# Performance work log

Measured on AMD Instinct MI355X. Metric: run time of the kernel, lower is better.

Reference implementation:

```python
import jax, jax.numpy as jnp
import numpy as np

B, T, E = 8, 2048, 1024
H = 16
HD = E // H            # per-head hidden_dim = 64
DFF = 4 * E
DC = T // 512          # decay_constant = 4
EPS = 1e-5


def setup_inputs() -> dict:
    key = jax.random.key(0)
    ks = jax.random.split(key, 8)
    return {
        "x": jax.random.normal(ks[0], (B, T, E), jnp.float32),
        # per-head input projections (Linear(dim, hidden_dim) x H)
        "w_proj": jax.random.normal(ks[1], (H, E, HD), jnp.float32) / np.sqrt(E),
        "b_proj": jnp.zeros((H, HD), jnp.float32),
        # causal mixing weights: first H//2 heads are Col-repeat, last H//2 Row-repeat
        "mix_w": jax.random.normal(ks[2], (H, T), jnp.float32),
        "mix_b": jnp.zeros((H, T), jnp.float32),
        "decay": jnp.ones((H,), jnp.float32),   # decay_value params (init ones as in torch)
        "out_w": jax.random.normal(ks[3], (E, E), jnp.float32) / np.sqrt(E),
        "out_b": jnp.zeros((E,), jnp.float32),
        "ln1_g": jnp.ones((E,), jnp.float32),
        "ln1_b": jnp.zeros((E,), jnp.float32),
        "ln2_g": jnp.ones((E,), jnp.float32),
        "ln2_b": jnp.zeros((E,), jnp.float32),
        "ff_w1": jax.random.normal(ks[4], (E, DFF), jnp.float32) / np.sqrt(E),
        "ff_b1": jnp.zeros((DFF,), jnp.float32),
        "ff_w2": jax.random.normal(ks[5], (DFF, E), jnp.float32) / np.sqrt(DFF),
        "ff_b2": jnp.zeros((E,), jnp.float32),
        "index": 0,
    }


def _layernorm(x, g, b):
    mu = jnp.mean(x, -1, keepdims=True)
    var = jnp.var(x, -1, keepdims=True)
    return (x - mu) * jax.lax.rsqrt(var + EPS) * g + b


def _mix_matrices(mix_w, decay):
    # Col heads: M[i,j] = v[j] * d**((j-i)/DC) for j>=i else 0
    # Row heads: M[i,j] = v[i] * d**((j-i)/DC) for j>=i else 0
    i = jnp.arange(T)[:, None]
    j = jnp.arange(T)[None, :]
    d = jnp.clip(decay, 0.9, 1.0)                                   # (H,)
    expo = (j - i).astype(jnp.float32) / DC                         # (T,T)
    dec = d[:, None, None] ** expo                                  # (H,T,T)
    causal = (j >= i)
    half = H // 2
    Mcol = jnp.where(causal, mix_w[:half, None, :] * dec[:half], 0.0)
    Mrow = jnp.where(causal, mix_w[half:, :, None] * dec[half:], 0.0)
    return jnp.concatenate([Mcol, Mrow], axis=0)                    # (H,T,T)


def reference(x, w_proj, b_proj, mix_w, mix_b, decay, out_w, out_b,
              ln1_g, ln1_b, ln2_g, ln2_b, ff_w1, ff_b1, ff_w2, ff_b2, index):
    # ---- token-mixing sub-block (parallel path of MixedRepeatHeads) ----
    res = x
    h = _layernorm(x, ln1_g, ln1_b)
    # per-head projection: (B,T,E) x (H,E,HD) -> (B,H,T,HD)
    p = jnp.einsum('bte,hef->bhtf', h, w_proj) + b_proj[:, None, :]
    M = _mix_matrices(mix_w, decay)
    # causal decay mixing along time: out[b,h,s,f] = sum_t p[b,h,t,f] * M[h,t,s]
    mixed = jnp.einsum('bhtf,hts->bhsf', p, M) + mix_b[None, :, :, None]
    # concat heads along feature dim -> (B,T,E)
    mixed = mixed.transpose(0, 2, 1, 3).reshape(B, T, E)
    mixed = mixed @ out_w + out_b
    x = mixed + res
    # ---- feed-forward sub-block ----
    res = x
    h = _layernorm(x, ln2_g, ln2_b)
    h = jax.nn.gelu(h @ ff_w1 + ff_b1) @ ff_w2 + ff_b2
    return h + res
```

## Files before the change

kernel.cpp:

```cpp
#include <hip/hip_runtime.h>


#define TT 2048
#define EE 1024
#define HHD 64
#define MROWS 16384
#define SC_L 64

typedef __bf16 bf16x8 __attribute__((ext_vector_type(8)));
typedef float f32x4 __attribute__((ext_vector_type(4)));
typedef unsigned short u16;
typedef unsigned int u32;
typedef u16 u16x8 __attribute__((ext_vector_type(8)));

__device__ __forceinline__ u16 f2bf(float f) {
  u32 u = __builtin_bit_cast(u32, f);
  u += 0x7FFFu + ((u >> 16) & 1u);
  return (u16)(u >> 16);
}
__device__ __forceinline__ float bf2f(u16 s) {
  u32 u = ((u32)s) << 16;
  return __builtin_bit_cast(float, u);
}
__device__ __forceinline__ float gelu_f(float x) {
  float x2 = x * x;
  float e = -1.5957691216057308f * x * __builtin_fmaf(0.044715f, x2, 1.0f);
  return x * __builtin_amdgcn_rcpf(1.0f + __expf(e));
}
__device__ __forceinline__ void gload_lds16(const void* g, void* l) {
  __builtin_amdgcn_global_load_lds(
      (const __attribute__((address_space(1))) u32*)g,
      (__attribute__((address_space(3))) u32*)l, 16, 0, 0);
}
__device__ __forceinline__ void wg_barrier() {
  asm volatile("" ::: "memory");
  __builtin_amdgcn_s_barrier();
  asm volatile("" ::: "memory");
}

__global__ __launch_bounds__(256) void transpose_to_bf16(
    const float* __restrict__ src, u16* __restrict__ dst, int R, int C,
    long sbs, long dbs) {
  __shared__ float tile[32][33];
  src += (long)blockIdx.z * sbs;
  dst += (long)blockIdx.z * dbs;
  int c0 = blockIdx.x * 32, r0 = blockIdx.y * 32;
  int tx = threadIdx.x, ty = threadIdx.y;
#pragma unroll
  for (int i = 0; i < 4; i++)
    tile[ty + i * 8][tx] = src[(long)(r0 + ty + i * 8) * C + c0 + tx];
  __syncthreads();
#pragma unroll
  for (int i = 0; i < 4; i++)
    dst[(long)(c0 + ty + i * 8) * R + r0 + tx] = f2bf(tile[tx][ty + i * 8]);
}

__global__ __launch_bounds__(256) void ln_to_bf16(
    const float* __restrict__ x, const float* __restrict__ gam,
    const float* __restrict__ bet, u16* __restrict__ y) {
  int row = blockIdx.x;
  int tid = threadIdx.x;
  float4 v = ((const float4*)x)[row * 256 + tid];
  float s = v.x + v.y + v.z + v.w;
  float s2 = v.x * v.x + v.y * v.y + v.z * v.z + v.w * v.w;
#pragma unroll
  for (int off = 1; off < 64; off <<= 1) {
    s += __shfl_xor(s, off);
    s2 += __shfl_xor(s2, off);
  }
  __shared__ float red[8];
  int w = tid >> 6;
  if ((tid & 63) == 0) { red[w] = s; red[4 + w] = s2; }
  __syncthreads();
  s = red[0] + red[1] + red[2] + red[3];
  s2 = red[4] + red[5] + red[6] + red[7];
  float mu = s * (1.0f / 1024.0f);
  float var = s2 * (1.0f / 1024.0f) - mu * mu;
  float rstd = rsqrtf(var + 1e-5f);
  int e0 = tid * 4;
  ushort4 o;
  o.x = f2bf((v.x - mu) * rstd * gam[e0 + 0] + bet[e0 + 0]);
  o.y = f2bf((v.y - mu) * rstd * gam[e0 + 1] + bet[e0 + 1]);
  o.z = f2bf((v.z - mu) * rstd * gam[e0 + 2] + bet[e0 + 2]);
  o.w = f2bf((v.w - mu) * rstd * gam[e0 + 3] + bet[e0 + 3]);
  ((ushort4*)y)[row * 256 + tid] = o;
}

template <int EPI>
__global__ __launch_bounds__(512, 1) void gemm256q(
    const u16* __restrict__ A, const u16* __restrict__ Bt,
    const float* __restrict__ bias, const float* __restrict__ res, void* outp,
    int M, int N, int K, int px, int gxp, int byper) {
  __shared__ u16 lds[65536];
  const int tid = threadIdx.x;
  const int w = tid >> 6, lane = tid & 63;
  const int wm = w >> 2, wn = w & 3;
  const int l15 = lane & 15, lk = lane >> 4;

  const int gx = (int)gridDim.x;
  const int bid = (int)blockIdx.y * gx + (int)blockIdx.x;
  const int xcd = bid & 7, i = bid >> 3;
  const int bx = (xcd % gxp) * px + (i % px);
  const int by = (xcd / gxp) * byper + (i / px);
  const int m0 = by * 256, n0 = bx * 256;

  const int srow = w * 16 + (lane >> 2);
  const int gslot = (lane & 3) ^ ((srow >> 1) & 3);
  const u16* aS = A + (size_t)(m0 + srow) * K + gslot * 8;
  const u16* aS2 = A + (size_t)(m0 + 128 + srow) * K +
                   (((lane & 3) ^ (((128 + srow) >> 1) & 3)) * 8);
  const u16* bS = Bt + (size_t)(n0 + srow) * K + gslot * 8;
  const u16* bS2 = Bt + (size_t)(n0 + 128 + srow) * K +
                   (((lane & 3) ^ (((128 + srow) >> 1) & 3)) * 8);

  f32x4 acc[8][4];
  const f32x4 z = {0.f, 0.f, 0.f, 0.f};
#pragma unroll
  for (int mi = 0; mi < 8; mi++)
#pragma unroll
    for (int ni = 0; ni < 4; ni++) acc[mi][ni] = z;

  const int sl = (lk ^ ((l15 >> 1) & 3)) * 8;
  const u32 ldsB = (u32)(uintptr_t)(void*)lds;
  const u32 aOffB = ldsB + (u32)(((wm * 128 + l15) * 32 + sl) * 2);
  const u32 bOffB = ldsB + 16384u + (u32)(((wn * 64 + l15) * 32 + sl) * 2);

#define STAGE(BUF, T_) { \
    u16* lb = lds + (BUF) * 16384 + w * 512; \
    const int kt = (T_) << 5; \
    gload_lds16(aS + kt, lb); \
    gload_lds16(aS2 + kt, lb + 4096); \
    gload_lds16(bS + kt, lb + 8192); \
    gload_lds16(bS2 + kt, lb + 12288); }

#define DS_RD(D, ADDR, OFF) \
    asm volatile("ds_read_b128 %0, %1 offset:" #OFF : "=v"(D) : "v"(ADDR))
#define WAITK(N_) { \
    asm volatile("s_waitcnt lgkmcnt(" #N_ ")" ::: "memory"); \
    __builtin_amdgcn_sched_barrier(0); }
#define MFMA4(MI, AF) { \
    acc[MI][0] = __builtin_amdgcn_mfma_f32_16x16x32_bf16(AF, bq0, acc[MI][0], 0, 0, 0); \
    acc[MI][1] = __builtin_amdgcn_mfma_f32_16x16x32_bf16(AF, bq1, acc[MI][1], 0, 0, 0); \
    acc[MI][2] = __builtin_amdgcn_mfma_f32_16x16x32_bf16(AF, bq2, acc[MI][2], 0, 0, 0); \
    acc[MI][3] = __builtin_amdgcn_mfma_f32_16x16x32_bf16(AF, bq3, acc[MI][3], 0, 0, 0); }

  const int nt = K >> 5;
  STAGE(0, 0);
  STAGE(1, 1);

  for (int t = 0; t < nt; ++t) {
    if (t + 2 < nt) {
      STAGE((t + 2) & 3, t + 2);
      asm volatile("s_waitcnt vmcnt(8)" ::: "memory");
    } else if (t + 1 < nt) {
      asm volatile("s_waitcnt vmcnt(4)" ::: "memory");
    } else {
      asm volatile("s_waitcnt vmcnt(0)" ::: "memory");
    }
    wg_barrier();

    const u32 bufO = (u32)(t & 3) * 32768u;
    const u32 aA = aOffB + bufO;
    const u32 bA = bOffB + bufO;
    bf16x8 bq0, bq1, bq2, bq3, af0, af1, af2, af3, af4, af5, af6, af7;
    DS_RD(bq0, bA, 0);
    DS_RD(bq1, bA, 1024);
    DS_RD(bq2, bA, 2048);
    DS_RD(bq3, bA, 3072);
    DS_RD(af0, aA, 0);
    DS_RD(af1, aA, 1024);
    DS_RD(af2, aA, 2048);
    DS_RD(af3, aA, 3072);
    DS_RD(af4, aA, 4096);
    DS_RD(af5, aA, 5120);
    DS_RD(af6, aA, 6144);
    DS_RD(af7, aA, 7168);
    WAITK(7);
    __builtin_amdgcn_s_setprio(1);
    MFMA4(0, af0);
    WAITK(6);
    MFMA4(1, af1);
    WAITK(5);
    MFMA4(2, af2);
    WAITK(4);
    MFMA4(3, af3);
    WAITK(3);
    MFMA4(4, af4);
    WAITK(2);
    MFMA4(5, af5);
    WAITK(1);
    MFMA4(6, af6);
    WAITK(0);
    MFMA4(7, af7);
    __builtin_amdgcn_s_setprio(0);
  }
#undef STAGE
#undef DS_RD
#undef WAITK
#undef MFMA4

#pragma unroll
  for (int mi = 0; mi < 8; mi++) {
#pragma unroll
    for (int ni = 0; ni < 4; ni++) {
      int n = n0 + wn * 64 + ni * 16 + l15;
      float bvv = bias[n];
#pragma unroll
      for (int r = 0; r < 4; r++) {
        int m = m0 + wm * 128 + mi * 16 + lk * 4 + r;
        size_t idx = (size_t)m * N + n;
        float v = acc[mi][ni][r] + bvv;
        if (EPI == 0) {
          ((u16*)outp)[idx] = f2bf(v);
        } else if (EPI == 1) {
          ((float*)outp)[idx] = v + res[idx];
        } else {
          ((u16*)outp)[idx] = f2bf(gelu_f(v));
        }
      }
    }
  }
}

__global__ __launch_bounds__(64) void scan_carry(
    const u16* __restrict__ p, const float* __restrict__ mix_w,
    const float* __restrict__ decay, float* __restrict__ carry) {
  int chunk = blockIdx.x * 8 + (threadIdx.x >> 3);
  int fg = threadIdx.x & 7;
  int c = chunk & 31, h = (chunk >> 5) & 15, b = chunk >> 9;
  float d = fminf(fmaxf(decay[h], 0.9f), 1.0f);
  float r = powf(d, 0.25f);
  size_t base = (((size_t)b * TT + c * SC_L) * EE + h * HHD + fg * 8) >> 3;
  const u16x8* p8 = (const u16x8*)p;
  const float* mw = mix_w + h * TT + c * SC_L;
  bool isRow = (h >= 8);
  float S[8] = {0.f, 0.f, 0.f, 0.f, 0.f, 0.f, 0.f, 0.f};
  for (int t = 0; t < SC_L; t++) {
    u16x8 v = p8[base + (size_t)t * (EE / 8)];
    float wv = isRow ? mw[t] : 1.0f;
#pragma unroll
    for (int j = 0; j < 8; j++) S[j] = r * S[j] + wv * bf2f(v[j]);
  }
  float* cp = carry + chunk * 64 + fg * 8;
#pragma unroll
  for (int j = 0; j < 8; j++) cp[j] = S[j];
}

__global__ __launch_bounds__(64) void scan_apply(
    const u16* __restrict__ p, const float* __restrict__ mix_w,
    const float* __restrict__ mix_b, const float* __restrict__ decay,
    const float* __restrict__ carry, u16* __restrict__ mixed) {
  int chunk = blockIdx.x * 8 + (threadIdx.x >> 3);
  int fg = threadIdx.x & 7;
  int c = chunk & 31, h = (chunk >> 5) & 15, b = chunk >> 9;
  float d = fminf(fmaxf(decay[h], 0.9f), 1.0f);
  float r = powf(d, 0.25f);
  float rl = powf(r, (float)SC_L);
  int cb = chunk - c;
  float S[8] = {0.f, 0.f, 0.f, 0.f, 0.f, 0.f, 0.f, 0.f};
  for (int cc = 0; cc < c; cc++) {
    const float* cp = carry + (cb + cc) * 64 + fg * 8;
#pragma unroll
    for (int j = 0; j < 8; j++) S[j] = rl * S[j] + cp[j];
  }
  size_t base = (((size_t)b * TT + c * SC_L) * EE + h * HHD + fg * 8) >> 3;
  const u16x8* p8 = (const u16x8*)p;
  u16x8* m8 = (u16x8*)mixed;
  const float* mw = mix_w + h * TT + c * SC_L;
  const float* mb = mix_b + h * TT + c * SC_L;
  bool isRow = (h >= 8);
  for (int t = 0; t < SC_L; t++) {
    u16x8 v = p8[base + (size_t)t * (EE / 8)];
    float wq = isRow ? mw[t] : 1.0f;
    float wo = isRow ? 1.0f : mw[t];
    float bb = mb[t];
    u16x8 o;
#pragma unroll
    for (int j = 0; j < 8; j++) {
      S[j] = r * S[j] + wq * bf2f(v[j]);
      o[j] = f2bf(wo * S[j] + bb);
    }
    m8[base + (size_t)t * (EE / 8)] = o;
  }
}

extern "C" void kernel_launch(void* const* d_in, const int* in_sizes, int n_in,
                              void* d_out, int out_size, void* d_ws, size_t ws_size,
                              hipStream_t stream) {
  const float* x = (const float*)d_in[0];
  const float* w_proj = (const float*)d_in[1];
  const float* b_proj = (const float*)d_in[2];
  const float* mix_w = (const float*)d_in[3];
  const float* mix_b = (const float*)d_in[4];
  const float* decay = (const float*)d_in[5];
  const float* out_w = (const float*)d_in[6];
  const float* out_b = (const float*)d_in[7];
  const float* ln1_g = (const float*)d_in[8];
  const float* ln1_b = (const float*)d_in[9];
  const float* ln2_g = (const float*)d_in[10];
  const float* ln2_b = (const float*)d_in[11];
  const float* ff_w1 = (const float*)d_in[12];
  const float* ff_b1 = (const float*)d_in[13];
  const float* ff_w2 = (const float*)d_in[14];
  const float* ff_b2 = (const float*)d_in[15];
  float* out = (float*)d_out;

  char* ws = (char*)d_ws;
  const size_t MiB = 1ull << 20;
  u16* wWp = (u16*)(ws + 0 * MiB);
  u16* wWo = (u16*)(ws + 2 * MiB);
  u16* wW1 = (u16*)(ws + 4 * MiB);
  u16* wW2 = (u16*)(ws + 12 * MiB);
  u16* wMix = (u16*)(ws + 20 * MiB);
  u16* wH = (u16*)(ws + 52 * MiB);
  u16* wP = (u16*)(ws + 84 * MiB);
  u16* wU = (u16*)(ws + 52 * MiB);
  float* wCarry = (float*)(ws + 180 * MiB);

  dim3 tb(32, 8);
  transpose_to_bf16<<<dim3(2, 32, 16), tb, 0, stream>>>(w_proj, wWp, 1024, 64,
                                                        65536L, 65536L);
  transpose_to_bf16<<<dim3(32, 32, 1), tb, 0, stream>>>(out_w, wWo, 1024, 1024, 0L, 0L);
  transpose_to_bf16<<<dim3(128, 32, 1), tb, 0, stream>>>(ff_w1, wW1, 1024, 4096, 0L, 0L);
  transpose_to_bf16<<<dim3(32, 128, 1), tb, 0, stream>>>(ff_w2, wW2, 4096, 1024, 0L, 0L);

  ln_to_bf16<<<dim3(MROWS), dim3(256), 0, stream>>>(x, ln1_g, ln1_b, wH);

  gemm256q<0><<<dim3(4, 64), dim3(512), 0, stream>>>(
      wH, wWp, b_proj, (const float*)nullptr, (void*)wP, MROWS, 1024, 1024,
      4, 1, 8);

  scan_carry<<<dim3(512), dim3(64), 0, stream>>>(wP, mix_w, decay, wCarry);
  scan_apply<<<dim3(512), dim3(64), 0, stream>>>(wP, mix_w, mix_b, decay, wCarry, wMix);

  gemm256q<1><<<dim3(4, 64), dim3(512), 0, stream>>>(
      wMix, wWo, out_b, x, (void*)out, MROWS, 1024, 1024,
      4, 1, 8);

  ln_to_bf16<<<dim3(MROWS), dim3(256), 0, stream>>>(out, ln2_g, ln2_b, wMix);

  gemm256q<2><<<dim3(16, 64), dim3(512), 0, stream>>>(
      wMix, wW1, ff_b1, (const float*)nullptr, (void*)wU, MROWS, 4096, 1024,
      4, 4, 32);

  gemm256q<1><<<dim3(4, 64), dim3(512), 0, stream>>>(
      wU, wW2, ff_b2, out, (void*)out, MROWS, 1024, 4096,
      2, 2, 16);
}
```

Baseline: 505.6 us.

## Shrink GEMM tile to 128x256 with double buffering for higher occupancy

Replaces the 256x256 GEMM tile with a 128x256 tile, halves the per-wave accumulator array, and cuts LDS use from 128 KiB to 48 KiB. The prefetch moves from a 4-buffer, 2-ahead scheme to 2-buffer double buffering with a second barrier per k-step, and launch bounds now allow several blocks per CU. The grids double in M and the XCD mapping parameters are rescaled to match. The aim is more resident waves to hide latency and better tail balance. The cost is lower arithmetic intensity per tile, more global and LDS traffic per FLOP, and an extra barrier on every iteration.

```diff
diff --git a/kernel.cpp b/kernel.cpp
--- a/kernel.cpp
+++ b/kernel.cpp
@@ -87,11 +87,11 @@
 }
 
 template <int EPI>
-__global__ __launch_bounds__(512, 1) void gemm256q(
+__global__ __launch_bounds__(512, 4) void gemm128n(
     const u16* __restrict__ A, const u16* __restrict__ Bt,
     const float* __restrict__ bias, const float* __restrict__ res, void* outp,
     int M, int N, int K, int px, int gxp, int byper) {
-  __shared__ u16 lds[65536];
+  __shared__ u16 lds[24576];
   const int tid = threadIdx.x;
   const int w = tid >> 6, lane = tid & 63;
   const int wm = w >> 2, wn = w & 3;
@@ -102,36 +102,32 @@
   const int xcd = bid & 7, i = bid >> 3;
   const int bx = (xcd % gxp) * px + (i % px);
   const int by = (xcd / gxp) * byper + (i / px);
-  const int m0 = by * 256, n0 = bx * 256;
+  const int m0 = by * 128, n0 = bx * 256;
 
   const int srow = w * 16 + (lane >> 2);
   const int gslot = (lane & 3) ^ ((srow >> 1) & 3);
   const u16* aS = A + (size_t)(m0 + srow) * K + gslot * 8;
-  const u16* aS2 = A + (size_t)(m0 + 128 + srow) * K +
-                   (((lane & 3) ^ (((128 + srow) >> 1) & 3)) * 8);
   const u16* bS = Bt + (size_t)(n0 + srow) * K + gslot * 8;
-  const u16* bS2 = Bt + (size_t)(n0 + 128 + srow) * K +
-                   (((lane & 3) ^ (((128 + srow) >> 1) & 3)) * 8);
-
-  f32x4 acc[8][4];
+  const u16* bS2 = Bt + (size_t)(n0 + 128 + srow) * K + gslot * 8;
+
+  f32x4 acc[4][4];
   const f32x4 z = {0.f, 0.f, 0.f, 0.f};
 #pragma unroll
-  for (int mi = 0; mi < 8; mi++)
+  for (int mi = 0; mi < 4; mi++)
 #pragma unroll
     for (int ni = 0; ni < 4; ni++) acc[mi][ni] = z;
 
   const int sl = (lk ^ ((l15 >> 1) & 3)) * 8;
   const u32 ldsB = (u32)(uintptr_t)(void*)lds;
-  const u32 aOffB = ldsB + (u32)(((wm * 128 + l15) * 32 + sl) * 2);
-  const u32 bOffB = ldsB + 16384u + (u32)(((wn * 64 + l15) * 32 + sl) * 2);
+  const u32 aOffB = ldsB + (u32)(((wm * 64 + l15) * 32 + sl) * 2);
+  const u32 bOffB = ldsB + 8192u + (u32)(((wn * 64 + l15) * 32 + sl) * 2);
 
 #define STAGE(BUF, T_) { \
-    u16* lb = lds + (BUF) * 16384 + w * 512; \
+    u16* lb = lds + (BUF) * 12288 + w * 512; \
     const int kt = (T_) << 5; \
     gload_lds16(aS + kt, lb); \
-    gload_lds16(aS2 + kt, lb + 4096); \
-    gload_lds16(bS + kt, lb + 8192); \
-    gload_lds16(bS2 + kt, lb + 12288); }
+    gload_lds16(bS + kt, lb + 4096); \
+    gload_lds16(bS2 + kt, lb + 8192); }
 
 #define DS_RD(D, ADDR, OFF) \
     asm volatile("ds_read_b128 %0, %1 offset:" #OFF : "=v"(D) : "v"(ADDR))
@@ -146,23 +142,20 @@
 
   const int nt = K >> 5;
   STAGE(0, 0);
-  STAGE(1, 1);
 
   for (int t = 0; t < nt; ++t) {
-    if (t + 2 < nt) {
-      STAGE((t + 2) & 3, t + 2);
-      asm volatile("s_waitcnt vmcnt(8)" ::: "memory");
-    } else if (t + 1 < nt) {
-      asm volatile("s_waitcnt vmcnt(4)" ::: "memory");
+    if (t + 1 < nt) {
+      STAGE((t + 1) & 1, t + 1);
+      asm volatile("s_waitcnt vmcnt(3)" ::: "memory");
     } else {
       asm volatile("s_waitcnt vmcnt(0)" ::: "memory");
     }
     wg_barrier();
 
-    const u32 bufO = (u32)(t & 3) * 32768u;
+    const u32 bufO = (u32)(t & 1) * 24576u;
     const u32 aA = aOffB + bufO;
     const u32 bA = bOffB + bufO;
-    bf16x8 bq0, bq1, bq2, bq3, af0, af1, af2, af3, af4, af5, af6, af7;
+    bf16x8 bq0, bq1, bq2, bq3, af0, af1, af2, af3;
     DS_RD(bq0, bA, 0);
     DS_RD(bq1, bA, 1024);
     DS_RD(bq2, bA, 2048);
@@ -171,28 +164,17 @@
     DS_RD(af1, aA, 1024);
     DS_RD(af2, aA, 2048);
     DS_RD(af3, aA, 3072);
-    DS_RD(af4, aA, 4096);
-    DS_RD(af5, aA, 5120);
-    DS_RD(af6, aA, 6144);
-    DS_RD(af7, aA, 7168);
-    WAITK(7);
+    WAITK(3);
     __builtin_amdgcn_s_setprio(1);
     MFMA4(0, af0);
-    WAITK(6);
+    WAITK(2);
     MFMA4(1, af1);
-    WAITK(5);
+    WAITK(1);
     MFMA4(2, af2);
-    WAITK(4);
+    WAITK(0);
     MFMA4(3, af3);
-    WAITK(3);
-    MFMA4(4, af4);
-    WAITK(2);
-    MFMA4(5, af5);
-    WAITK(1);
-    MFMA4(6, af6);
-    WAITK(0);
-    MFMA4(7, af7);
     __builtin_amdgcn_s_setprio(0);
+    wg_barrier();
   }
 #undef STAGE
 #undef DS_RD
@@ -200,14 +182,14 @@
 #undef MFMA4
 
 #pragma unroll
-  for (int mi = 0; mi < 8; mi++) {
+  for (int mi = 0; mi < 4; mi++) {
 #pragma unroll
     for (int ni = 0; ni < 4; ni++) {
       int n = n0 + wn * 64 + ni * 16 + l15;
       float bvv = bias[n];
 #pragma unroll
       for (int r = 0; r < 4; r++) {
-        int m = m0 + wm * 128 + mi * 16 + lk * 4 + r;
+        int m = m0 + wm * 64 + mi * 16 + lk * 4 + r;
         size_t idx = (size_t)m * N + n;
         float v = acc[mi][ni][r] + bvv;
         if (EPI == 0) {
@@ -326,24 +308,24 @@
 
   ln_to_bf16<<<dim3(MROWS), dim3(256), 0, stream>>>(x, ln1_g, ln1_b, wH);
 
-  gemm256q<0><<<dim3(4, 64), dim3(512), 0, stream>>>(
+  gemm128n<0><<<dim3(4, 128), dim3(512), 0, stream>>>(
       wH, wWp, b_proj, (const float*)nullptr, (void*)wP, MROWS, 1024, 1024,
-      4, 1, 8);
+      4, 1, 16);
 
   scan_carry<<<dim3(512), dim3(64), 0, stream>>>(wP, mix_w, decay, wCarry);
   scan_apply<<<dim3(512), dim3(64), 0, stream>>>(wP, mix_w, mix_b, decay, wCarry, wMix);
 
-  gemm256q<1><<<dim3(4, 64), dim3(512), 0, stream>>>(
+  gemm128n<1><<<dim3(4, 128), dim3(512), 0, stream>>>(
       wMix, wWo, out_b, x, (void*)out, MROWS, 1024, 1024,
-      4, 1, 8);
+      4, 1, 16);
 
   ln_to_bf16<<<dim3(MROWS), dim3(256), 0, stream>>>(out, ln2_g, ln2_b, wMix);
 
-  gemm256q<2><<<dim3(16, 64), dim3(512), 0, stream>>>(
+  gemm128n<2><<<dim3(16, 128), dim3(512), 0, stream>>>(
       wMix, wW1, ff_b1, (const float*)nullptr, (void*)wU, MROWS, 4096, 1024,
-      4, 4, 32);
-
-  gemm256q<1><<<dim3(4, 64), dim3(512), 0, stream>>>(
+      4, 4, 64);
+
+  gemm128n<1><<<dim3(4, 128), dim3(512), 0, stream>>>(
       wU, wW2, ff_b2, out, (void*)out, MROWS, 1024, 4096,
-      2, 2, 16);
-}
+      2, 2, 32);
+}
```

Measured after the change: 535.1 us. +5.8%, slower.
